# Performance work log

Measured on AMD Instinct MI355X. Metric: run time of the kernel, lower is better.

The kernel has to match this reference:

```python
import jax, jax.numpy as jnp
import numpy as np

B, N, NIN = 8, 1024, 64
CTX = 3            # context window -> concat dim = NIN*CTX = 192
H = 128            # hidden layer size
NOUT = 2


def _shift_down(x, d):
    # torch: z[:, d:, :] = x[:, :-d, :]
    return jnp.pad(x[:, :-d, :], ((0, 0), (d, 0), (0, 0)))


def _shift_up(x, d):
    # torch: z[:, :-d, :] = x[:, d:, :]
    return jnp.pad(x[:, d:, :], ((0, 0), (0, d), (0, 0)))


def setup_inputs() -> dict:
    key = jax.random.key(0)
    ks = jax.random.split(key, 8)
    n = NIN * CTX  # 192
    s1 = 1.0 / np.sqrt(n)
    s2 = 1.0 / np.sqrt(H)
    return {
        "x_l": jax.random.normal(ks[0], (B, N, NIN), dtype=jnp.float32),
        "W_l": jax.random.uniform(ks[1], (H, n), jnp.float32, -s1, s1),
        "b_l": jax.random.uniform(ks[2], (H,), jnp.float32, -s1, s1),
        "W_r": jax.random.uniform(ks[3], (H, n), jnp.float32, -s1, s1),
        "b_r": jax.random.uniform(ks[4], (H,), jnp.float32, -s1, s1),
        "W_bil": jax.random.uniform(ks[5], (NOUT, H, H), jnp.float32, -s2, s2),
        "b_bil": jax.random.uniform(ks[6], (NOUT,), jnp.float32, -s2, s2),
    }


def reference(x_l, W_l, b_l, W_r, b_r, W_bil, b_bil):
    x_r = x_l  # forward called with x_r=None
    # context expansion (context=3 -> d=1 only): order matches torch append order
    z_l = [x_l]
    z_r = [x_r]
    for d in range(1, CTX // 2 + 1):
        z_l.append(_shift_down(x_l, d)); z_r.append(_shift_up(x_r, d))
        z_l.append(_shift_up(x_l, d));   z_r.append(_shift_down(x_r, d))
    xl = jnp.concatenate(z_l, axis=2)  # [B,N,NIN*CTX]
    xr = jnp.concatenate(z_r, axis=2)
    # MLP (single hidden layer, relu; dropout_rate=0 -> identity)
    hl = jax.nn.relu(jnp.einsum('bnf,hf->bnh', xl, W_l) + b_l)  # [B,N,H]
    hr = jax.nn.relu(jnp.einsum('bnf,hf->bnh', xr, W_r) + b_r)  # [B,N,H]
    # bilinear pairwise score without materializing the expanded [B*N*N,H] tensors
    t = jnp.einsum('bih,khg->bikg', hl, W_bil)                  # [B,N,NOUT,H]
    out = jnp.einsum('bikg,bjg->bijk', t, hr) + b_bil           # [B,N,N,NOUT]
    return out
```

## Files before the change

kernel.cpp:

```cpp
#include <hip/hip_runtime.h>
#include <hip/hip_bf16.h>

typedef __attribute__((ext_vector_type(8))) __bf16 bf16x8;
typedef __attribute__((ext_vector_type(4))) float f32x4;

#define DEVI static __device__ __forceinline__

DEVI unsigned short f2bf(float f) {
    union { float f; unsigned int u; } v; v.f = f;
    unsigned int u = v.u;
    u += 0x7FFFu + ((u >> 16) & 1u);
    return (unsigned short)(u >> 16);
}

__global__ void prep_kernel(const float* __restrict__ Wl,
                            const float* __restrict__ Wr,
                            const float* __restrict__ Wb,
                            unsigned short* __restrict__ WcatT,
                            unsigned short* __restrict__ WtT)
{
    int i = blockIdx.x * 256 + threadIdx.x;
    const int TOT = 256*192 + 256*128;
    if (i >= TOT) return;
    if (i < 256*192) {
        int c = i / 192, kk = i % 192;
        float v;
        if (c < 128) {
            int orig = (kk < 64) ? (kk + 64) : ((kk < 128) ? (kk - 64) : kk);
            v = Wl[c*192 + orig];
        } else {
            int orig = (kk < 64) ? (kk + 128) : (kk - 64);
            v = Wr[(c-128)*192 + orig];
        }
        WcatT[i] = f2bf(v);
    } else {
        int j = i - 256*192;
        int c = j >> 7, h = j & 127;
        int k = c >> 7, g = c & 127;
        WtT[j] = f2bf(Wb[(k*128 + h)*128 + g]);
    }
}

__global__ __launch_bounds__(256) void stage1_kernel(
    const float* __restrict__ x,
    const float* __restrict__ bl,
    const float* __restrict__ br,
    const unsigned short* __restrict__ WcatT,
    const unsigned short* __restrict__ WtT,
    unsigned short* __restrict__ t_out,
    unsigned short* __restrict__ hr_out)
{
    __shared__ unsigned short xwin[34*72];
    __shared__ unsigned short Hbuf[32*264];
    __shared__ unsigned short Tbuf[32*264];

    const int tid = threadIdx.x;
    const int blk = blockIdx.x;
    const int b   = blk >> 5;
    const int n0  = (blk & 31) << 5;

    for (int c = tid; c < 34*16; c += 256) {
        int row = c >> 4, ch = c & 15;
        int n = n0 - 1 + row;
        float4 v = make_float4(0.f, 0.f, 0.f, 0.f);
        if (n >= 0 && n < 1024)
            v = ((const float4*)(x + ((size_t)b*1024 + n)*64))[ch];
        unsigned short* d = &xwin[row*72 + ch*4];
        d[0]=f2bf(v.x); d[1]=f2bf(v.y); d[2]=f2bf(v.z); d[3]=f2bf(v.w);
    }
    __syncthreads();

    const int lane = tid & 63, wave = tid >> 6;
    const int q = lane >> 4, m = lane & 15;

    bf16x8 a[2][6];
    #pragma unroll
    for (int rs = 0; rs < 2; ++rs)
        #pragma unroll
        for (int ks = 0; ks < 6; ++ks) {
            int row = rs*16 + m;
            int k = ks*32 + q*8;
            a[rs][ks] = *(const bf16x8*)&xwin[(row + (k >> 6))*72 + (k & 63)];
        }

    #pragma unroll
    for (int cs = 0; cs < 4; ++cs) {
        const int c0 = (wave*4 + cs)*16;
        bf16x8 bw[6];
        #pragma unroll
        for (int ks = 0; ks < 6; ++ks)
            bw[ks] = *(const bf16x8*)(WcatT + (size_t)(c0 + m)*192 + ks*32 + q*8);
        f32x4 acc0 = {0.f,0.f,0.f,0.f}, acc1 = {0.f,0.f,0.f,0.f};
        #pragma unroll
        for (int ks = 0; ks < 6; ++ks) {
            acc0 = __builtin_amdgcn_mfma_f32_16x16x32_bf16(a[0][ks], bw[ks], acc0, 0, 0, 0);
            acc1 = __builtin_amdgcn_mfma_f32_16x16x32_bf16(a[1][ks], bw[ks], acc1, 0, 0, 0);
        }
        const int c = c0 + m;
        const float bias = (c < 128) ? bl[c] : br[c - 128];
        #pragma unroll
        for (int r = 0; r < 4; ++r) {
            Hbuf[(q*4 + r)*264 + c]      = f2bf(fmaxf(acc0[r] + bias, 0.f));
            Hbuf[(16 + q*4 + r)*264 + c] = f2bf(fmaxf(acc1[r] + bias, 0.f));
        }
    }
    __syncthreads();

    for (int c = tid; c < 512; c += 256) {
        int row = c >> 4, ch = c & 15;
        bf16x8 v = *(const bf16x8*)&Hbuf[row*264 + 128 + ch*8];
        *(bf16x8*)(hr_out + ((size_t)(b*1024 + n0 + row))*128 + ch*8) = v;
    }

    bf16x8 a2[2][4];
    #pragma unroll
    for (int rs = 0; rs < 2; ++rs)
        #pragma unroll
        for (int ks = 0; ks < 4; ++ks)
            a2[rs][ks] = *(const bf16x8*)&Hbuf[(rs*16 + m)*264 + ks*32 + q*8];

    #pragma unroll
    for (int cs = 0; cs < 4; ++cs) {
        const int c0 = (wave*4 + cs)*16;
        bf16x8 bw[4];
        #pragma unroll
        for (int ks = 0; ks < 4; ++ks)
            bw[ks] = *(const bf16x8*)(WtT + (size_t)(c0 + m)*128 + ks*32 + q*8);
        f32x4 acc0 = {0.f,0.f,0.f,0.f}, acc1 = {0.f,0.f,0.f,0.f};
        #pragma unroll
        for (int ks = 0; ks < 4; ++ks) {
            acc0 = __builtin_amdgcn_mfma_f32_16x16x32_bf16(a2[0][ks], bw[ks], acc0, 0, 0, 0);
            acc1 = __builtin_amdgcn_mfma_f32_16x16x32_bf16(a2[1][ks], bw[ks], acc1, 0, 0, 0);
        }
        const int c = c0 + m;
        #pragma unroll
        for (int r = 0; r < 4; ++r) {
            Tbuf[(q*4 + r)*264 + c]      = f2bf(acc0[r]);
            Tbuf[(16 + q*4 + r)*264 + c] = f2bf(acc1[r]);
        }
    }
    __syncthreads();

    for (int c = tid; c < 1024; c += 256) {
        int row = c >> 5, ch = c & 31;
        bf16x8 v = *(const bf16x8*)&Tbuf[row*264 + ch*8];
        *(bf16x8*)(t_out + ((size_t)(b*1024 + n0 + row))*256 + ch*8) = v;
    }
}

__global__ __launch_bounds__(256) void stage2_kernel(
    const unsigned short* __restrict__ t_in,
    const unsigned short* __restrict__ hr_in,
    const float* __restrict__ bbil,
    float* __restrict__ out)
{
    const int b = blockIdx.z;
    const int tid = threadIdx.x, lane = tid & 63, wave = tid >> 6;
    const int q = lane >> 4, m = lane & 15;
    const int i0 = blockIdx.y*64 + (wave & 1)*32;
    const int j0 = blockIdx.x*128 + (wave >> 1)*64;

    const unsigned short* tb = t_in  + (size_t)b*1024*256;
    const unsigned short* hb = hr_in + (size_t)b*1024*128;

    f32x4 acc[2][2][4];
    #pragma unroll
    for (int ch = 0; ch < 2; ++ch)
        #pragma unroll
        for (int is = 0; is < 2; ++is)
            #pragma unroll
            for (int js = 0; js < 4; ++js)
                acc[ch][is][js] = (f32x4){0.f,0.f,0.f,0.f};

    #pragma unroll
    for (int ks = 0; ks < 4; ++ks) {
        bf16x8 af[2][2], bf[4];
        #pragma unroll
        for (int is = 0; is < 2; ++is) {
            const unsigned short* rp = tb + (size_t)(i0 + is*16 + m)*256 + ks*32 + q*8;
            af[0][is] = *(const bf16x8*)(rp);
            af[1][is] = *(const bf16x8*)(rp + 128);
        }
        #pragma unroll
        for (int js = 0; js < 4; ++js)
            bf[js] = *(const bf16x8*)(hb + (size_t)(j0 + js*16 + m)*128 + ks*32 + q*8);

        #pragma unroll
        for (int ch = 0; ch < 2; ++ch)
            #pragma unroll
            for (int is = 0; is < 2; ++is)
                #pragma unroll
                for (int js = 0; js < 4; ++js)
                    acc[ch][is][js] = __builtin_amdgcn_mfma_f32_16x16x32_bf16(
                        af[ch][is], bf[js], acc[ch][is][js], 0, 0, 0);
    }

    const float bb0 = bbil[0], bb1 = bbil[1];
    #pragma unroll
    for (int is = 0; is < 2; ++is)
        #pragma unroll
        for (int js = 0; js < 4; ++js)
            #pragma unroll
            for (int r = 0; r < 4; ++r) {
                int i = i0 + is*16 + q*4 + r;
                int j = j0 + js*16 + m;
                float2 v = make_float2(acc[0][is][js][r] + bb0,
                                       acc[1][is][js][r] + bb1);
                *(float2*)(out + ((size_t)(b*1024 + i)*1024 + j)*2) = v;
            }
}

extern "C" void kernel_launch(void* const* d_in, const int* in_sizes, int n_in,
                              void* d_out, int out_size, void* d_ws, size_t ws_size,
                              hipStream_t stream)
{
    const float* x    = (const float*)d_in[0];
    const float* Wl   = (const float*)d_in[1];
    const float* bl   = (const float*)d_in[2];
    const float* Wr   = (const float*)d_in[3];
    const float* br   = (const float*)d_in[4];
    const float* Wb   = (const float*)d_in[5];
    const float* bbil = (const float*)d_in[6];
    float* out = (float*)d_out;

    unsigned char* ws = (unsigned char*)d_ws;
    unsigned short* t_ws  = (unsigned short*)(ws);
    unsigned short* hr_ws = (unsigned short*)(ws + (4u<<20));
    unsigned short* WcatT = (unsigned short*)(ws + (6u<<20));
    unsigned short* WtT   = (unsigned short*)(ws + (6u<<20) + 98304);

    prep_kernel<<<320, 256, 0, stream>>>(Wl, Wr, Wb, WcatT, WtT);
    stage1_kernel<<<256, 256, 0, stream>>>(x, bl, br, WcatT, WtT, t_ws, hr_ws);
    stage2_kernel<<<dim3(8, 16, 8), 256, 0, stream>>>(t_ws, hr_ws, bbil, out);
}
```

Before: 114.9 us.

## Halve stage1 row tile, swap stage2 grid order, use nontemporal output stores

```diff
diff --git a/kernel.cpp b/kernel.cpp
--- a/kernel.cpp
+++ b/kernel.cpp
@@ -3,6 +3,7 @@
 
 typedef __attribute__((ext_vector_type(8))) __bf16 bf16x8;
 typedef __attribute__((ext_vector_type(4))) float f32x4;
+typedef __attribute__((ext_vector_type(2))) float f32x2;
 
 #define DEVI static __device__ __forceinline__
 
@@ -50,16 +51,16 @@
     unsigned short* __restrict__ t_out,
     unsigned short* __restrict__ hr_out)
 {
-    __shared__ unsigned short xwin[34*72];
-    __shared__ unsigned short Hbuf[32*264];
-    __shared__ unsigned short Tbuf[32*264];
+    __shared__ unsigned short xwin[18*72];
+    __shared__ unsigned short Hbuf[16*264];
+    __shared__ unsigned short Tbuf[16*264];
 
     const int tid = threadIdx.x;
     const int blk = blockIdx.x;
-    const int b   = blk >> 5;
-    const int n0  = (blk & 31) << 5;
-
-    for (int c = tid; c < 34*16; c += 256) {
+    const int b   = blk >> 6;
+    const int n0  = (blk & 63) << 4;
+
+    for (int c = tid; c < 18*16; c += 256) {
         int row = c >> 4, ch = c & 15;
         int n = n0 - 1 + row;
         float4 v = make_float4(0.f, 0.f, 0.f, 0.f);
@@ -73,15 +74,12 @@
     const int lane = tid & 63, wave = tid >> 6;
     const int q = lane >> 4, m = lane & 15;
 
-    bf16x8 a[2][6];
-    #pragma unroll
-    for (int rs = 0; rs < 2; ++rs)
-        #pragma unroll
-        for (int ks = 0; ks < 6; ++ks) {
-            int row = rs*16 + m;
-            int k = ks*32 + q*8;
-            a[rs][ks] = *(const bf16x8*)&xwin[(row + (k >> 6))*72 + (k & 63)];
-        }
+    bf16x8 a[6];
+    #pragma unroll
+    for (int ks = 0; ks < 6; ++ks) {
+        int k = ks*32 + q*8;
+        a[ks] = *(const bf16x8*)&xwin[(m + (k >> 6))*72 + (k & 63)];
+    }
 
     #pragma unroll
     for (int cs = 0; cs < 4; ++cs) {
@@ -90,34 +88,28 @@
         #pragma unroll
         for (int ks = 0; ks < 6; ++ks)
             bw[ks] = *(const bf16x8*)(WcatT + (size_t)(c0 + m)*192 + ks*32 + q*8);
-        f32x4 acc0 = {0.f,0.f,0.f,0.f}, acc1 = {0.f,0.f,0.f,0.f};
-        #pragma unroll
-        for (int ks = 0; ks < 6; ++ks) {
-            acc0 = __builtin_amdgcn_mfma_f32_16x16x32_bf16(a[0][ks], bw[ks], acc0, 0, 0, 0);
-            acc1 = __builtin_amdgcn_mfma_f32_16x16x32_bf16(a[1][ks], bw[ks], acc1, 0, 0, 0);
-        }
+        f32x4 acc0 = {0.f,0.f,0.f,0.f};
+        #pragma unroll
+        for (int ks = 0; ks < 6; ++ks)
+            acc0 = __builtin_amdgcn_mfma_f32_16x16x32_bf16(a[ks], bw[ks], acc0, 0, 0, 0);
         const int c = c0 + m;
         const float bias = (c < 128) ? bl[c] : br[c - 128];
         #pragma unroll
-        for (int r = 0; r < 4; ++r) {
-            Hbuf[(q*4 + r)*264 + c]      = f2bf(fmaxf(acc0[r] + bias, 0.f));
-            Hbuf[(16 + q*4 + r)*264 + c] = f2bf(fmaxf(acc1[r] + bias, 0.f));
-        }
+        for (int r = 0; r < 4; ++r)
+            Hbuf[(q*4 + r)*264 + c] = f2bf(fmaxf(acc0[r] + bias, 0.f));
     }
     __syncthreads();
 
-    for (int c = tid; c < 512; c += 256) {
-        int row = c >> 4, ch = c & 15;
+    {
+        int row = tid >> 4, ch = tid & 15;
         bf16x8 v = *(const bf16x8*)&Hbuf[row*264 + 128 + ch*8];
         *(bf16x8*)(hr_out + ((size_t)(b*1024 + n0 + row))*128 + ch*8) = v;
     }
 
-    bf16x8 a2[2][4];
-    #pragma unroll
-    for (int rs = 0; rs < 2; ++rs)
-        #pragma unroll
-        for (int ks = 0; ks < 4; ++ks)
-            a2[rs][ks] = *(const bf16x8*)&Hbuf[(rs*16 + m)*264 + ks*32 + q*8];
+    bf16x8 a2[4];
+    #pragma unroll
+    for (int ks = 0; ks < 4; ++ks)
+        a2[ks] = *(const bf16x8*)&Hbuf[m*264 + ks*32 + q*8];
 
     #pragma unroll
     for (int cs = 0; cs < 4; ++cs) {
@@ -126,22 +118,18 @@
         #pragma unroll
         for (int ks = 0; ks < 4; ++ks)
             bw[ks] = *(const bf16x8*)(WtT + (size_t)(c0 + m)*128 + ks*32 + q*8);
-        f32x4 acc0 = {0.f,0.f,0.f,0.f}, acc1 = {0.f,0.f,0.f,0.f};
-        #pragma unroll
-        for (int ks = 0; ks < 4; ++ks) {
-            acc0 = __builtin_amdgcn_mfma_f32_16x16x32_bf16(a2[0][ks], bw[ks], acc0, 0, 0, 0);
-            acc1 = __builtin_amdgcn_mfma_f32_16x16x32_bf16(a2[1][ks], bw[ks], acc1, 0, 0, 0);
-        }
+        f32x4 acc0 = {0.f,0.f,0.f,0.f};
+        #pragma unroll
+        for (int ks = 0; ks < 4; ++ks)
+            acc0 = __builtin_amdgcn_mfma_f32_16x16x32_bf16(a2[ks], bw[ks], acc0, 0, 0, 0);
         const int c = c0 + m;
         #pragma unroll
-        for (int r = 0; r < 4; ++r) {
-            Tbuf[(q*4 + r)*264 + c]      = f2bf(acc0[r]);
-            Tbuf[(16 + q*4 + r)*264 + c] = f2bf(acc1[r]);
-        }
+        for (int r = 0; r < 4; ++r)
+            Tbuf[(q*4 + r)*264 + c] = f2bf(acc0[r]);
     }
     __syncthreads();
 
-    for (int c = tid; c < 1024; c += 256) {
+    for (int c = tid; c < 512; c += 256) {
         int row = c >> 5, ch = c & 31;
         bf16x8 v = *(const bf16x8*)&Tbuf[row*264 + ch*8];
         *(bf16x8*)(t_out + ((size_t)(b*1024 + n0 + row))*256 + ch*8) = v;
@@ -157,8 +145,8 @@
     const int b = blockIdx.z;
     const int tid = threadIdx.x, lane = tid & 63, wave = tid >> 6;
     const int q = lane >> 4, m = lane & 15;
-    const int i0 = blockIdx.y*64 + (wave & 1)*32;
-    const int j0 = blockIdx.x*128 + (wave >> 1)*64;
+    const int i0 = blockIdx.x*64 + (wave & 1)*32;
+    const int j0 = blockIdx.y*128 + (wave >> 1)*64;
 
     const unsigned short* tb = t_in  + (size_t)b*1024*256;
     const unsigned short* hb = hr_in + (size_t)b*1024*128;
@@ -204,9 +192,9 @@
             for (int r = 0; r < 4; ++r) {
                 int i = i0 + is*16 + q*4 + r;
                 int j = j0 + js*16 + m;
-                float2 v = make_float2(acc[0][is][js][r] + bb0,
-                                       acc[1][is][js][r] + bb1);
-                *(float2*)(out + ((size_t)(b*1024 + i)*1024 + j)*2) = v;
+                f32x2 v = { acc[0][is][js][r] + bb0, acc[1][is][js][r] + bb1 };
+                __builtin_nontemporal_store(
+                    v, (f32x2*)(out + ((size_t)(b*1024 + i)*1024 + j)*2));
             }
 }
 
@@ -230,6 +218,6 @@
     unsigned short* WtT   = (unsigned short*)(ws + (6u<<20) + 98304);
 
     prep_kernel<<<320, 256, 0, stream>>>(Wl, Wr, Wb, WcatT, WtT);
-    stage1_kernel<<<256, 256, 0, stream>>>(x, bl, br, WcatT, WtT, t_ws, hr_ws);
-    stage2_kernel<<<dim3(8, 16, 8), 256, 0, stream>>>(t_ws, hr_ws, bbil, out);
-}
+    stage1_kernel<<<512, 256, 0, stream>>>(x, bl, br, WcatT, WtT, t_ws, hr_ws);
+    stage2_kernel<<<dim3(16, 8, 8), 256, 0, stream>>>(t_ws, hr_ws, bbil, out);
+}
```

Result: slower. 117.9 us (+2.6%).
